# Performance work log

Hardware: AMD Instinct MI355X
Metric: run time of the kernel (lower is better)

## Reference

```python
import jax, jax.numpy as jnp
import numpy as np

N_HEAD = 16
EPS = 1e-5


def setup_inputs() -> dict:
    key = jax.random.key(0)
    ks = jax.random.split(key, 9)
    B, T, C = 2, 1024, 1024
    s = 0.02
    return {
        "x": jax.random.normal(ks[0], (B, T, C), jnp.float32),
        "Wq": jax.random.normal(ks[1], (C, C), jnp.float32) * s,
        "Wk": jax.random.normal(ks[2], (C, C), jnp.float32) * s,
        "Wv": jax.random.normal(ks[3], (C, C), jnp.float32) * s,
        "Wq2": jax.random.normal(ks[4], (C, C), jnp.float32) * s,
        "Wk2": jax.random.normal(ks[5], (C, C), jnp.float32) * s,
        "Wo": jax.random.normal(ks[6], (C, C), jnp.float32) * s,
        "mixture": jnp.full((1,), -5.0, jnp.float32),  # quartet_gate_init
        "quartet_scale": jnp.ones((1,), jnp.float32),
    }


def reference(x, Wq, Wk, Wv, Wq2, Wk2, Wo, mixture, quartet_scale):
    B, T, C = x.shape
    H = N_HEAD
    Dh = C // H
    scale = 1.0 / jnp.sqrt(jnp.asarray(Dh, x.dtype))

    def heads(W):
        # torch Linear: y = x @ W.T ; then view(B,T,H,Dh).transpose(1,2)
        return (x @ W.T).reshape(B, T, H, Dh).transpose(0, 2, 1, 3)  # [B,H,T,Dh]

    q, k, v = heads(Wq), heads(Wk), heads(Wv)
    q2, k2 = heads(Wq2), heads(Wk2)

    qk = jnp.einsum("bhqd,bhkd->bhqk", q, k) * scale      # [B,H,T,T]
    q2k2 = jnp.einsum("bhqd,bhkd->bhqk", q2, k2) * scale  # [B,H,T,T]

    def row_norm(s):
        mu = s.mean(axis=-1, keepdims=True)
        sigma = s.std(axis=-1, keepdims=True, ddof=1)  # torch std is unbiased
        return (s - mu) / (sigma + EPS)

    qk_n = row_norm(qk)
    q2k2_n = row_norm(q2k2)
    m = jax.nn.sigmoid(mixture)  # [1], broadcasts
    scores = (1.0 - m) * qk_n + m * (qk_n * q2k2_n) * quartet_scale

    causal = jnp.tril(jnp.ones((T, T), bool))  # [T,T]
    scores = jnp.where(causal, scores, -jnp.inf)
    attn = jax.nn.softmax(scores, axis=-1)  # [B,H,T,T]

    y = jnp.einsum("bhqk,bhkd->bhqd", attn, v)  # [B,H,T,Dh]
    y = y.transpose(0, 2, 1, 3).reshape(B, T, C)
    return y @ Wo.T
```

## Files before the change

kernel.cpp:

```cpp
#include <hip/hip_runtime.h>
#include <hip/hip_bf16.h>
#include <stdint.h>

#define TS 1024
#define CS 1024
#define NH 16
#define DHEAD 64
#define NBATCH 2
#define EPSV 1e-5f
#define MEG 1048576

typedef __bf16 bf16x8 __attribute__((ext_vector_type(8)));
typedef float  f32x4  __attribute__((ext_vector_type(4)));

#define MFMA(a, b, c) __builtin_amdgcn_mfma_f32_16x16x32_bf16((a), (b), (c), 0, 0, 0)

__device__ __forceinline__ float bf2f(ushort u){
  union { uint32_t i; float f; } v; v.i = ((uint32_t)u) << 16; return v.f;
}
__device__ __forceinline__ ushort f2bf(float f){
  union { float f; uint32_t i; } v; v.f = f;
  uint32_t r = v.i + 0x7FFFu + ((v.i >> 16) & 1u);
  return (ushort)(r >> 16);
}

__device__ __forceinline__ void gl_lds16(const ushort* g, ushort* l) {
  __builtin_amdgcn_global_load_lds(
      (const __attribute__((address_space(1))) void*)g,
      (__attribute__((address_space(3))) void*)l, 16, 0, 0);
}

__global__ __launch_bounds__(256)
void cast_all(const float* __restrict__ x,
              const float* __restrict__ Wq, const float* __restrict__ Wk,
              const float* __restrict__ Wv, const float* __restrict__ Wq2,
              const float* __restrict__ Wk2, const float* __restrict__ Wo,
              ushort* __restrict__ xb, ushort* __restrict__ wcat)
{
  const int XC = 524288, TOT = 2097152;
  for (int idx = blockIdx.x * 256 + threadIdx.x; idx < TOT; idx += 524288) {
    const float* s; ushort* d; int c;
    if (idx < XC) { s = x; d = xb; c = idx; }
    else {
      int r = idx - XC; int w = r >> 18; c = r & 262143;
      switch (w) {
        case 0:  s = Wq;  d = wcat;           break;
        case 1:  s = Wk;  d = wcat + 1*MEG;   break;
        case 2:  s = Wv;  d = wcat + 4*MEG;   break;
        case 3:  s = Wq2; d = wcat + 2*MEG;   break;
        case 4:  s = Wk2; d = wcat + 3*MEG;   break;
        default: s = Wo;  d = wcat + 5*MEG;   break;
      }
    }
    float4 v = *(const float4*)(s + (size_t)c * 4);
    ushort4 o; o.x = f2bf(v.x); o.y = f2bf(v.y); o.z = f2bf(v.z); o.w = f2bf(v.w);
    *(ushort4*)(d + (size_t)c * 4) = o;
  }
}

#define BN 128

__global__ __launch_bounds__(256, 2)
void gemm_proj(const ushort* __restrict__ A, const ushort* __restrict__ Bt,
               ushort* __restrict__ qb, ushort* __restrict__ kb,
               ushort* __restrict__ q2b, ushort* __restrict__ k2b,
               ushort* __restrict__ vtb,
               ushort* __restrict__ ktb, ushort* __restrict__ k2tb)
{
  __shared__ ushort a_s[64 * 64];
  __shared__ ushort b_s[128 * 64];

  const int bid = blockIdx.x;
  const int s   = (bid & 7) * 160 + (bid >> 3);
  const int n0  = (s >> 5) * BN;
  const int m0  = (s & 31) * 64;

  const int t  = threadIdx.x;
  const int w  = t >> 6, l = t & 63;
  const int wr = w >> 1, wc = w & 1;
  const int l15 = l & 15, l4 = l >> 4;
  const int r8 = l >> 3, g7 = l & 7;

  f32x4 acc[2][4] = {};

  for (int k0 = 0; k0 < CS; k0 += 64) {
    #pragma unroll
    for (int i = 0; i < 2; ++i) {
      int issue = w * 2 + i;
      int row   = issue * 8 + r8;
      int gs    = g7 ^ (row & 7);
      gl_lds16(&A[(size_t)(m0 + row) * CS + k0 + gs * 8], &a_s[issue * 512]);
    }
    #pragma unroll
    for (int i = 0; i < 4; ++i) {
      int issue = w * 4 + i;
      int row   = issue * 8 + r8;
      int gs    = g7 ^ (row & 7);
      gl_lds16(&Bt[(size_t)(n0 + row) * CS + k0 + gs * 8], &b_s[issue * 512]);
    }
    __syncthreads();

    #pragma unroll
    for (int ks = 0; ks < 2; ++ks) {
      bf16x8 af[2], bfr[4];
      #pragma unroll
      for (int mi = 0; mi < 2; ++mi) {
        int row = wr * 32 + mi * 16 + l15;
        int gl  = (ks * 4 + l4) ^ (row & 7);
        af[mi] = *(const bf16x8*)&a_s[row * 64 + gl * 8];
      }
      #pragma unroll
      for (int ni = 0; ni < 4; ++ni) {
        int row = wc * 64 + ni * 16 + l15;
        int gl  = (ks * 4 + l4) ^ (row & 7);
        bfr[ni] = *(const bf16x8*)&b_s[row * 64 + gl * 8];
      }
      #pragma unroll
      for (int mi = 0; mi < 2; ++mi)
        #pragma unroll
        for (int ni = 0; ni < 4; ++ni)
          acc[mi][ni] = MFMA(af[mi], bfr[ni], acc[mi][ni]);
    }

    __syncthreads();
  }

  #pragma unroll
  for (int mi = 0; mi < 2; ++mi) {
    #pragma unroll
    for (int ni = 0; ni < 4; ++ni) {
      int col  = n0 + wc * 64 + ni * 16 + l15;
      int row0 = m0 + wr * 32 + mi * 16 + l4 * 4;
      int seg  = col >> 10, cc = col & (CS - 1);
      if (seg < 4) {
        ushort* dst = (seg == 0) ? qb : (seg == 1) ? kb : (seg == 2) ? q2b : k2b;
        float sc = (seg & 1) ? 1.f : 0.125f;
        #pragma unroll
        for (int e = 0; e < 4; ++e)
          dst[(size_t)(row0 + e) * CS + cc] = f2bf(acc[mi][ni][e] * sc);
        if (seg == 1 || seg == 3) {
          int bb = row0 >> 10, tt = row0 & (TS - 1);
          int hh = cc >> 6, dd = cc & (DHEAD - 1);
          ushort* td = (seg == 1) ? ktb : k2tb;
          ushort4 o;
          o.x = f2bf(acc[mi][ni][0]); o.y = f2bf(acc[mi][ni][1]);
          o.z = f2bf(acc[mi][ni][2]); o.w = f2bf(acc[mi][ni][3]);
          *(ushort4*)&td[(((size_t)(bb * NH + hh) * DHEAD + dd) * TS) + tt] = o;
        }
      } else {
        int bb = row0 >> 10, tt = row0 & (TS - 1);
        int hh = cc >> 6, dd = cc & (DHEAD - 1);
        ushort4 o;
        o.x = f2bf(acc[mi][ni][0]); o.y = f2bf(acc[mi][ni][1]);
        o.z = f2bf(acc[mi][ni][2]); o.w = f2bf(acc[mi][ni][3]);
        *(ushort4*)&vtb[(((size_t)(bb * NH + hh) * DHEAD + dd) * TS) + tt] = o;
      }
    }
  }
}

__global__ __launch_bounds__(256, 2)
void gemm_out(const ushort* __restrict__ A, const ushort* __restrict__ Bt,
              float* __restrict__ C)
{
  __shared__ ushort a_s[64 * 64];
  __shared__ ushort b_s[64 * 64];

  const int bid = blockIdx.x;
  const int s   = (bid & 7) * 64 + (bid >> 3);
  const int n0  = (s >> 5) * 64;
  const int m0  = (s & 31) * 64;

  const int t  = threadIdx.x;
  const int w  = t >> 6, l = t & 63;
  const int wr = w >> 1, wc = w & 1;
  const int l15 = l & 15, l4 = l >> 4;
  const int r8 = l >> 3, g7 = l & 7;

  f32x4 acc[2][2] = {};

  for (int k0 = 0; k0 < CS; k0 += 64) {
    #pragma unroll
    for (int i = 0; i < 2; ++i) {
      int issue = w * 2 + i;
      int row   = issue * 8 + r8;
      int gs    = g7 ^ (row & 7);
      gl_lds16(&A [(size_t)(m0 + row) * CS + k0 + gs * 8], &a_s[issue * 512]);
      gl_lds16(&Bt[(size_t)(n0 + row) * CS + k0 + gs * 8], &b_s[issue * 512]);
    }
    __syncthreads();

    #pragma unroll
    for (int ks = 0; ks < 2; ++ks) {
      bf16x8 af[2], bfr[2];
      #pragma unroll
      for (int mi = 0; mi < 2; ++mi) {
        int row = wr * 32 + mi * 16 + l15;
        int gl  = (ks * 4 + l4) ^ (row & 7);
        af[mi] = *(const bf16x8*)&a_s[row * 64 + gl * 8];
      }
      #pragma unroll
      for (int ni = 0; ni < 2; ++ni) {
        int row = wc * 32 + ni * 16 + l15;
        int gl  = (ks * 4 + l4) ^ (row & 7);
        bfr[ni] = *(const bf16x8*)&b_s[row * 64 + gl * 8];
      }
      #pragma unroll
      for (int mi = 0; mi < 2; ++mi)
        #pragma unroll
        for (int ni = 0; ni < 2; ++ni)
          acc[mi][ni] = MFMA(af[mi], bfr[ni], acc[mi][ni]);
    }

    __syncthreads();
  }

  #pragma unroll
  for (int mi = 0; mi < 2; ++mi)
    #pragma unroll
    for (int ni = 0; ni < 2; ++ni)
      #pragma unroll
      for (int e = 0; e < 4; ++e)
        C[(size_t)(m0 + wr * 32 + mi * 16 + l4 * 4 + e) * CS +
          n0 + wc * 32 + ni * 16 + l15] = acc[mi][ni][e];
}

__global__ __launch_bounds__(256, 2)
void gram(const ushort* __restrict__ ktb, const ushort* __restrict__ k2tb,
          ushort* __restrict__ g1b, ushort* __restrict__ g2b,
          float* __restrict__ csb)
{
  __shared__ ushort t_s[64 * 128];

  const int mat = blockIdx.x & 1, z = blockIdx.x >> 1;
  const ushort* S = (mat ? k2tb : ktb) + (size_t)z * DHEAD * TS;

  const int t = threadIdx.x, w = t >> 6, l = t & 63;
  const int l15 = l & 15, l4 = l >> 4;

  f32x4 acc[4] = {};
  float csacc = 0.f;

  for (int tt = 0; tt < 8; ++tt) {
    const int t0 = tt * 128;
    __syncthreads();
    #pragma unroll
    for (int i = 0; i < 4; ++i) {
      int issue = w * 4 + i;
      int row = issue * 4 + l4;
      int gs  = l15 ^ (row & 15);
      gl_lds16(&S[(size_t)row * TS + t0 + gs * 8], &t_s[issue * 512]);
    }
    __syncthreads();

    {
      int r = w * 16 + l15;
      #pragma unroll
      for (int j = 0; j < 4; ++j) {
        int gg = ((l4 * 4 + j) ^ (r & 15)) * 8;
        uint4 vv = *(const uint4*)&t_s[r * 128 + gg];
        const ushort* pu = (const ushort*)&vv;
        #pragma unroll
        for (int e2 = 0; e2 < 8; ++e2) csacc += bf2f(pu[e2]);
      }
    }

    #pragma unroll
    for (int ks = 0; ks < 4; ++ks) {
      int ar = w * 16 + l15;
      bf16x8 af = *(const bf16x8*)&t_s[ar * 128 + ((ks * 4 + l4) ^ (ar & 15)) * 8];
      #pragma unroll
      for (int ni = 0; ni < 4; ++ni) {
        int br = ni * 16 + l15;
        bf16x8 bf_ = *(const bf16x8*)&t_s[br * 128 + ((ks * 4 + l4) ^ (br & 15)) * 8];
        acc[ni] = MFMA(af, bf_, acc[ni]);
      }
    }
  }

  csacc += __shfl_xor(csacc, 16);
  csacc += __shfl_xor(csacc, 32);
  if (l4 == 0)
    csb[(mat * 32 + z) * 64 + w * 16 + l15] = csacc;

  ushort* G = (mat ? g2b : g1b) + (size_t)z * 4096;
  #pragma unroll
  for (int ni = 0; ni < 4; ++ni)
    #pragma unroll
    for (int e = 0; e < 4; ++e)
      G[(w * 16 + l4 * 4 + e) * 64 + ni * 16 + l15] = f2bf(acc[ni][e]);
}

__global__ __launch_bounds__(256, 3)
void attn_fused(const ushort* __restrict__ qb, const ushort* __restrict__ kb,
                const ushort* __restrict__ q2b, const ushort* __restrict__ k2b,
                const ushort* __restrict__ vtb, ushort* __restrict__ yb,
                const ushort* __restrict__ g1b, const ushort* __restrict__ g2b,
                const float* __restrict__ csb,
                const float* __restrict__ mixture, const float* __restrict__ qsc)
{
  __shared__ ushort kbuf [2][4096];
  __shared__ ushort k2buf[2][4096];
  __shared__ ushort vbuf [2][4096];
  __shared__ ushort p_s  [2 * 32 * 40];

  const int idx  = blockIdx.x;
  const int pp   = idx >> 8;
  const int base = idx & 255;
  const int xcd  = base & 7;
  const int mm   = base >> 3;
  const int qq   = mm & 7;
  const int z    = (mm >> 3) * 8 + xcd;
  const int q32  = (pp == 0) ? (31 - qq) : (pp == 1) ? qq
                 : (pp == 2) ? (23 - qq) : (8 + qq);
  const int b    = z >> 4, h = z & 15;
  const int m0   = q32 * 32;
  const int nkv  = (q32 >> 1) + 1;

  const ushort* Q  = qb  + (size_t)b * TS * CS + h * DHEAD;
  const ushort* Q2 = q2b + (size_t)b * TS * CS + h * DHEAD;
  const ushort* K  = kb  + (size_t)b * TS * CS + h * DHEAD;
  const ushort* K2 = k2b + (size_t)b * TS * CS + h * DHEAD;
  const ushort* Vt = vtb + (size_t)z * DHEAD * TS;
  const ushort* G1 = g1b + (size_t)z * 4096;
  const ushort* G2 = g2b + (size_t)z * 4096;
  ushort* Y = yb + (size_t)b * TS * CS + h * DHEAD;

  const int t = threadIdx.x, w = t >> 6, l = t & 63;
  const int l15 = l & 15, l4 = l >> 4;
  const int r8 = l >> 3, g7 = l & 7;
  const int p  = w >> 1, wr = w & 1;
  const int qrow = wr * 16 + l15;

  const float L2E = 1.44269504f;
  const float gm = 1.f / (1.f + __expf(-mixture[0]));
  const float mq2 = gm * qsc[0] * L2E;
  const float om2 = (1.f - gm) * L2E;

  auto stage_k = [&](int ti, int bs) {
    const int t0 = ti * 64;
    #pragma unroll
    for (int i = 0; i < 2; ++i) {
      int issue = w * 2 + i;
      int row = issue * 8 + r8;
      int gs  = g7 ^ (row & 7);
      gl_lds16(&K [(size_t)(t0 + row) * CS + gs * 8], &kbuf [bs][issue * 512]);
      gl_lds16(&K2[(size_t)(t0 + row) * CS + gs * 8], &k2buf[bs][issue * 512]);
    }
  };
  auto stage_v = [&](int ti, int bs) {
    const int t0 = ti * 64;
    #pragma unroll
    for (int i = 0; i < 2; ++i) {
      int issue = w * 2 + i;
      int row = issue * 8 + r8;
      int gs  = g7 ^ (row & 7);
      gl_lds16(&Vt[(size_t)row * TS + t0 + gs * 8], &vbuf[bs][issue * 512]);
    }
  };

  {
    int row = w * 8 + r8;
    int gs  = g7 ^ (row & 7);
    gl_lds16(&Q [(size_t)(m0 + row) * CS + gs * 8], &p_s[w * 512]);
    gl_lds16(&Q2[(size_t)(m0 + row) * CS + gs * 8], &kbuf[1][w * 512]);
  }
  stage_k(0, 0);
  stage_v(0, 0);
  __syncthreads();

  bf16x8 fq[2], fq2[2];
  #pragma unroll
  for (int ks = 0; ks < 2; ++ks) {
    int gg = ((ks * 4 + l4) ^ (qrow & 7)) * 8;
    fq [ks] = *(const bf16x8*)&p_s[qrow * 64 + gg];
    fq2[ks] = *(const bf16x8*)&kbuf[1][qrow * 64 + gg];
  }

  f32x4 U1[4] = {}, U2[4] = {};
  #pragma unroll
  for (int ks = 0; ks < 2; ++ks)
    #pragma unroll
    for (int ni = 0; ni < 4; ++ni) {
      bf16x8 bg = *(const bf16x8*)&G1[(ni * 16 + l15) * 64 + ks * 32 + l4 * 8];
      U1[ni] = MFMA(bg, fq[ks], U1[ni]);
    }
  #pragma unroll
  for (int ks = 0; ks < 2; ++ks)
    #pragma unroll
    for (int ni = 0; ni < 4; ++ni) {
      bf16x8 bg = *(const bf16x8*)&G2[(ni * 16 + l15) * 64 + ks * 32 + l4 * 8];
      U2[ni] = MFMA(bg, fq2[ks], U2[ni]);
    }

  float ssq1 = 0.f, md1 = 0.f, ssq2 = 0.f, md2 = 0.f;
  #pragma unroll
  for (int ni = 0; ni < 4; ++ni) {
    int gsq = (ni * 2 + (l4 >> 1)) ^ (qrow & 7);
    int off = qrow * 64 + gsq * 8 + (l4 & 1) * 4;
    ushort qa[4], qb2[4];
    *(uint2*)qa  = *(const uint2*)&p_s[off];
    *(uint2*)qb2 = *(const uint2*)&kbuf[1][off];
    float c1[4], c2[4];
    *(float4*)c1 = *(const float4*)&csb[z * 64 + ni * 16 + l4 * 4];
    *(float4*)c2 = *(const float4*)&csb[2048 + z * 64 + ni * 16 + l4 * 4];
    #pragma unroll
    for (int e = 0; e < 4; ++e) {
      float qv1 = bf2f(qa[e]), qv2 = bf2f(qb2[e]);
      ssq1 = fmaf(U1[ni][e], qv1, ssq1); md1 = fmaf(qv1, c1[e], md1);
      ssq2 = fmaf(U2[ni][e], qv2, ssq2); md2 = fmaf(qv2, c2[e], md2);
    }
  }
  ssq1 += __shfl_xor(ssq1, 16); md1 += __shfl_xor(md1, 16);
  ssq2 += __shfl_xor(ssq2, 16); md2 += __shfl_xor(md2, 16);
  ssq1 += __shfl_xor(ssq1, 32); md1 += __shfl_xor(md1, 32);
  ssq2 += __shfl_xor(ssq2, 32); md2 += __shfl_xor(md2, 32);

  const float mu1 = md1 * (1.f / TS), mu2 = md2 * (1.f / TS);
  const float va1 = (ssq1 - (float)TS * mu1 * mu1) * (1.f / (TS - 1));
  const float va2 = (ssq2 - (float)TS * mu2 * mu2) * (1.f / (TS - 1));
  const float iv1 = 1.f / (sqrtf(fmaxf(va1, 0.f)) + EPSV);
  const float iv2 = 1.f / (sqrtf(fmaxf(va2, 0.f)) + EPSV);
  __syncthreads();

  float lrow = 0.f;
  f32x4 accO[4] = {};

  for (int i = 0; i < nkv; ++i) {
    const int t0  = i * 64;
    const int cur = i & 1;
    if (i + 1 < nkv) { stage_k(i + 1, cur ^ 1); stage_v(i + 1, cur ^ 1); }

    const ushort* ks_ = kbuf [cur];
    const ushort* k2s_= k2buf[cur];

    f32x4 a1[2] = {}, a2[2] = {};
    #pragma unroll
    for (int ks = 0; ks < 2; ++ks) {
      bf16x8 bk[2], bk2[2];
      #pragma unroll
      for (int ni = 0; ni < 2; ++ni) {
        int j  = p * 32 + ni * 16 + l15;
        int gg = ((ks * 4 + l4) ^ (j & 7)) * 8;
        bk [ni] = *(const bf16x8*)&ks_ [j * 64 + gg];
        bk2[ni] = *(const bf16x8*)&k2s_[j * 64 + gg];
      }
      #pragma unroll
      for (int ni = 0; ni < 2; ++ni) {
        a1[ni] = MFMA(bk [ni], fq [ks], a1[ni]);
        a2[ni] = MFMA(bk2[ni], fq2[ks], a2[ni]);
      }
    }

    const int grow = m0 + qrow;
    #pragma unroll
    for (int ni = 0; ni < 2; ++ni) {
      float pe[4];
      #pragma unroll
      for (int e = 0; e < 4; ++e) {
        float n1 = (a1[ni][e] - mu1) * iv1;
        float n2 = (a2[ni][e] - mu2) * iv2;
        float sc = n1 * fmaf(mq2, n2, om2);
        float pv = exp2f(sc);
        int gcol = t0 + p * 32 + ni * 16 + l4 * 4 + e;
        pv = (gcol <= grow) ? pv : 0.f;
        lrow += pv;
        pe[e] = pv;
      }
      uint32_t pk01, pk23;
      asm("v_cvt_pk_bf16_f32 %0, %1, %2" : "=v"(pk01) : "v"(pe[0]), "v"(pe[1]));
      asm("v_cvt_pk_bf16_f32 %0, %1, %2" : "=v"(pk23) : "v"(pe[2]), "v"(pe[3]));
      uint2 pk; pk.x = pk01; pk.y = pk23;
      *(uint2*)&p_s[p * 1280 + qrow * 40 + ni * 16 + l4 * 4] = pk;
    }

    {
      bf16x8 ap = *(const bf16x8*)&p_s[p * 1280 + qrow * 40 + l4 * 8];
      #pragma unroll
      for (int ni = 0; ni < 4; ++ni) {
        int d  = ni * 16 + l15;
        int gg = ((p * 4 + l4) ^ (d & 7)) * 8;
        bf16x8 bv = *(const bf16x8*)&vbuf[cur][d * 64 + gg];
        accO[ni] = MFMA(ap, bv, accO[ni]);
      }
    }

    __syncthreads();
  }

  lrow += __shfl_xor(lrow, 16);
  lrow += __shfl_xor(lrow, 32);

  float* fb = (float*)kbuf;
  float* fl = (float*)k2buf;
  if (p == 1) {
    #pragma unroll
    for (int ni = 0; ni < 4; ++ni)
      #pragma unroll
      for (int e = 0; e < 4; ++e)
        fb[(wr * 16 + l4 * 4 + e) * 64 + ni * 16 + l15] = accO[ni][e];
    if (l4 == 0) fl[qrow] = lrow;
  }
  __syncthreads();
  if (p == 0) {
    float lt = lrow + fl[qrow];
    float il[4];
    #pragma unroll
    for (int e = 0; e < 4; ++e)
      il[e] = 1.f / __shfl(lt, l4 * 4 + e);
    #pragma unroll
    for (int ni = 0; ni < 4; ++ni)
      #pragma unroll
      for (int e = 0; e < 4; ++e) {
        float o = accO[ni][e] + fb[(wr * 16 + l4 * 4 + e) * 64 + ni * 16 + l15];
        Y[(size_t)(m0 + wr * 16 + l4 * 4 + e) * CS + ni * 16 + l15] = f2bf(o * il[e]);
      }
  }
}

extern "C" void kernel_launch(void* const* d_in, const int* in_sizes, int n_in,
                              void* d_out, int out_size, void* d_ws, size_t ws_size,
                              hipStream_t stream) {
  const float* x    = (const float*)d_in[0];
  const float* Wq   = (const float*)d_in[1];
  const float* Wk   = (const float*)d_in[2];
  const float* Wv   = (const float*)d_in[3];
  const float* Wq2  = (const float*)d_in[4];
  const float* Wk2  = (const float*)d_in[5];
  const float* Wo   = (const float*)d_in[6];
  const float* mixture = (const float*)d_in[7];
  const float* qsc  = (const float*)d_in[8];
  float* out = (float*)d_out;

  ushort* ws = (ushort*)d_ws;
  ushort* xb   = ws;
  ushort* wcat = xb   + (size_t)2 * MEG;
  ushort* qb   = wcat + (size_t)6 * MEG;
  ushort* q2b  = qb   + (size_t)2 * MEG;
  ushort* kb   = q2b  + (size_t)2 * MEG;
  ushort* k2b  = kb   + (size_t)2 * MEG;
  ushort* vtb  = k2b  + (size_t)2 * MEG;
  ushort* yb   = vtb  + (size_t)2 * MEG;
  ushort* ktb  = yb   + (size_t)2 * MEG;
  ushort* k2tb = ktb  + (size_t)2 * MEG;
  ushort* g1b  = k2tb + (size_t)2 * MEG;
  ushort* g2b  = g1b  + (size_t)(MEG / 8);
  float*  csb  = (float*)(g2b + (size_t)(MEG / 8));
  ushort* wob  = wcat + (size_t)5 * MEG;

  cast_all<<<2048, 256, 0, stream>>>(x, Wq, Wk, Wv, Wq2, Wk2, Wo, xb, wcat);

  gemm_proj<<<1280, 256, 0, stream>>>(
      xb, wcat, qb, kb, q2b, k2b, vtb, ktb, k2tb);

  gram<<<64, 256, 0, stream>>>(ktb, k2tb, g1b, g2b, csb);

  attn_fused<<<1024, 256, 0, stream>>>(qb, kb, q2b, k2b, vtb, yb,
                                       g1b, g2b, csb, mixture, qsc);

  gemm_out<<<512, 256, 0, stream>>>(yb, wob, out);
}
```

Measured before the change: 105.5 us.

## Load K2 fragments directly into registers, drop K2 LDS staging

K2 tiles are no longer staged through shared memory; each wave loads its MFMA fragments straight from global memory into a double-buffered register set, and the KV loop is unrolled by two so the register buffers alternate statically. This cuts LDS footprint by a third, which can raise occupancy, and removes the LDS reads for K2. In exchange it raises register pressure and uses uncoalesced-ish direct global loads whose latency must be hidden by one tile of compute.

```diff
diff --git a/kernel.cpp b/kernel.cpp
--- a/kernel.cpp
+++ b/kernel.cpp
@@ -299,10 +299,9 @@
                 const float* __restrict__ csb,
                 const float* __restrict__ mixture, const float* __restrict__ qsc)
 {
-  __shared__ ushort kbuf [2][4096];
-  __shared__ ushort k2buf[2][4096];
-  __shared__ ushort vbuf [2][4096];
-  __shared__ ushort p_s  [2 * 32 * 40];
+  __shared__ ushort kbuf[2][4096];
+  __shared__ ushort vbuf[2][4096];
+  __shared__ ushort p_s [2 * 32 * 40];
 
   const int idx  = blockIdx.x;
   const int pp   = idx >> 8;
@@ -344,8 +343,7 @@
       int issue = w * 2 + i;
       int row = issue * 8 + r8;
       int gs  = g7 ^ (row & 7);
-      gl_lds16(&K [(size_t)(t0 + row) * CS + gs * 8], &kbuf [bs][issue * 512]);
-      gl_lds16(&K2[(size_t)(t0 + row) * CS + gs * 8], &k2buf[bs][issue * 512]);
+      gl_lds16(&K[(size_t)(t0 + row) * CS + gs * 8], &kbuf[bs][issue * 512]);
     }
   };
   auto stage_v = [&](int ti, int bs) {
@@ -359,6 +357,18 @@
     }
   };
 
+  bf16x8 k2A[2][2], k2B[2][2];
+#define LOAD_K2(ti, dst)                                                        \
+  {                                                                             \
+    const int t0_ = (ti) * 64;                                                  \
+    _Pragma("unroll")                                                           \
+    for (int ni = 0; ni < 2; ++ni)                                              \
+      _Pragma("unroll")                                                         \
+      for (int ks = 0; ks < 2; ++ks)                                            \
+        dst[ni][ks] = *(const bf16x8*)&K2[(size_t)(t0_ + p * 32 + ni * 16 + l15)\
+                                          * CS + ks * 32 + l4 * 8];             \
+  }
+
   {
     int row = w * 8 + r8;
     int gs  = g7 ^ (row & 7);
@@ -367,6 +377,7 @@
   }
   stage_k(0, 0);
   stage_v(0, 0);
+  LOAD_K2(0, k2A);
   __syncthreads();
 
   bf16x8 fq[2], fq2[2];
@@ -426,73 +437,82 @@
   float lrow = 0.f;
   f32x4 accO[4] = {};
 
-  for (int i = 0; i < nkv; ++i) {
-    const int t0  = i * 64;
-    const int cur = i & 1;
-    if (i + 1 < nkv) { stage_k(i + 1, cur ^ 1); stage_v(i + 1, cur ^ 1); }
-
-    const ushort* ks_ = kbuf [cur];
-    const ushort* k2s_= k2buf[cur];
-
-    f32x4 a1[2] = {}, a2[2] = {};
-    #pragma unroll
-    for (int ks = 0; ks < 2; ++ks) {
-      bf16x8 bk[2], bk2[2];
-      #pragma unroll
-      for (int ni = 0; ni < 2; ++ni) {
-        int j  = p * 32 + ni * 16 + l15;
-        int gg = ((ks * 4 + l4) ^ (j & 7)) * 8;
-        bk [ni] = *(const bf16x8*)&ks_ [j * 64 + gg];
-        bk2[ni] = *(const bf16x8*)&k2s_[j * 64 + gg];
-      }
-      #pragma unroll
-      for (int ni = 0; ni < 2; ++ni) {
-        a1[ni] = MFMA(bk [ni], fq [ks], a1[ni]);
-        a2[ni] = MFMA(bk2[ni], fq2[ks], a2[ni]);
-      }
-    }
-
-    const int grow = m0 + qrow;
-    #pragma unroll
-    for (int ni = 0; ni < 2; ++ni) {
-      float pe[4];
-      #pragma unroll
-      for (int e = 0; e < 4; ++e) {
-        float n1 = (a1[ni][e] - mu1) * iv1;
-        float n2 = (a2[ni][e] - mu2) * iv2;
-        float sc = n1 * fmaf(mq2, n2, om2);
-        float pv = exp2f(sc);
-        int gcol = t0 + p * 32 + ni * 16 + l4 * 4 + e;
-        pv = (gcol <= grow) ? pv : 0.f;
-        lrow += pv;
-        pe[e] = pv;
-      }
-      uint32_t pk01, pk23;
-      asm("v_cvt_pk_bf16_f32 %0, %1, %2" : "=v"(pk01) : "v"(pe[0]), "v"(pe[1]));
-      asm("v_cvt_pk_bf16_f32 %0, %1, %2" : "=v"(pk23) : "v"(pe[2]), "v"(pe[3]));
-      uint2 pk; pk.x = pk01; pk.y = pk23;
-      *(uint2*)&p_s[p * 1280 + qrow * 40 + ni * 16 + l4 * 4] = pk;
-    }
-
-    {
-      bf16x8 ap = *(const bf16x8*)&p_s[p * 1280 + qrow * 40 + l4 * 8];
-      #pragma unroll
-      for (int ni = 0; ni < 4; ++ni) {
-        int d  = ni * 16 + l15;
-        int gg = ((p * 4 + l4) ^ (d & 7)) * 8;
-        bf16x8 bv = *(const bf16x8*)&vbuf[cur][d * 64 + gg];
-        accO[ni] = MFMA(ap, bv, accO[ni]);
-      }
-    }
-
-    __syncthreads();
-  }
+#define COMPUTE_TILE(ti, KS_, VS_, K2F)                                         \
+  {                                                                             \
+    const int t0 = (ti) * 64;                                                   \
+    f32x4 a1[2] = {}, a2[2] = {};                                               \
+    _Pragma("unroll")                                                           \
+    for (int ks = 0; ks < 2; ++ks) {                                            \
+      bf16x8 bk[2];                                                             \
+      _Pragma("unroll")                                                         \
+      for (int ni = 0; ni < 2; ++ni) {                                          \
+        int j  = p * 32 + ni * 16 + l15;                                        \
+        int gg = ((ks * 4 + l4) ^ (j & 7)) * 8;                                 \
+        bk[ni] = *(const bf16x8*)&KS_[j * 64 + gg];                             \
+      }                                                                         \
+      _Pragma("unroll")                                                         \
+      for (int ni = 0; ni < 2; ++ni) {                                          \
+        a1[ni] = MFMA(bk[ni], fq[ks], a1[ni]);                                  \
+        a2[ni] = MFMA(K2F[ni][ks], fq2[ks], a2[ni]);                            \
+      }                                                                         \
+    }                                                                           \
+    const int grow = m0 + qrow;                                                 \
+    _Pragma("unroll")                                                           \
+    for (int ni = 0; ni < 2; ++ni) {                                            \
+      float pe[4];                                                              \
+      _Pragma("unroll")                                                         \
+      for (int e = 0; e < 4; ++e) {                                             \
+        float n1 = (a1[ni][e] - mu1) * iv1;                                     \
+        float n2 = (a2[ni][e] - mu2) * iv2;                                     \
+        float sc = n1 * fmaf(mq2, n2, om2);                                     \
+        float pv = exp2f(sc);                                                   \
+        int gcol = t0 + p * 32 + ni * 16 + l4 * 4 + e;                          \
+        pv = (gcol <= grow) ? pv : 0.f;                                         \
+        lrow += pv;                                                             \
+        pe[e] = pv;                                                             \
+      }                                                                         \
+      uint32_t pk01, pk23;                                                      \
+      asm("v_cvt_pk_bf16_f32 %0, %1, %2" : "=v"(pk01) : "v"(pe[0]), "v"(pe[1]));\
+      asm("v_cvt_pk_bf16_f32 %0, %1, %2" : "=v"(pk23) : "v"(pe[2]), "v"(pe[3]));\
+      uint2 pk; pk.x = pk01; pk.y = pk23;                                       \
+      *(uint2*)&p_s[p * 1280 + qrow * 40 + ni * 16 + l4 * 4] = pk;              \
+    }                                                                           \
+    {                                                                           \
+      bf16x8 ap = *(const bf16x8*)&p_s[p * 1280 + qrow * 40 + l4 * 8];          \
+      _Pragma("unroll")                                                         \
+      for (int ni = 0; ni < 4; ++ni) {                                          \
+        int d  = ni * 16 + l15;                                                 \
+        int gg = ((p * 4 + l4) ^ (d & 7)) * 8;                                  \
+        bf16x8 bv = *(const bf16x8*)&VS_[d * 64 + gg];                          \
+        accO[ni] = MFMA(ap, bv, accO[ni]);                                      \
+      }                                                                         \
+    }                                                                           \
+  }
+
+  for (int ii = 0; ii < nkv; ii += 2) {
+    if (ii + 1 < nkv) {
+      stage_k(ii + 1, 1); stage_v(ii + 1, 1);
+      LOAD_K2(ii + 1, k2B);
+    }
+    COMPUTE_TILE(ii, kbuf[0], vbuf[0], k2A);
+    __syncthreads();
+    if (ii + 1 >= nkv) break;
+
+    if (ii + 2 < nkv) {
+      stage_k(ii + 2, 0); stage_v(ii + 2, 0);
+      LOAD_K2(ii + 2, k2A);
+    }
+    COMPUTE_TILE(ii + 1, kbuf[1], vbuf[1], k2B);
+    __syncthreads();
+  }
+#undef COMPUTE_TILE
+#undef LOAD_K2
 
   lrow += __shfl_xor(lrow, 16);
   lrow += __shfl_xor(lrow, 32);
 
   float* fb = (float*)kbuf;
-  float* fl = (float*)k2buf;
+  float* fl = (float*)vbuf;
   if (p == 1) {
     #pragma unroll
     for (int ni = 0; ni < 4; ++ni)
```

Result: no change. 104.8 us (-0.6%).

## Use 64-row query tiles per attention block, dropping the KV split-reduction

Applied to the files above, without the earlier changes.

Each attention block now covers 64 query rows, one 16-row slice per wave, over the full 64-column KV tile, where before it covered 32 rows split across two wave pairs that each took half the KV columns. This halves the grid and removes the final cross-wave reduction through shared memory and its extra barrier. It also halves K/K2/V loads per query row, since each staged tile now serves twice as many rows. In exchange each wave holds twice the score accumulators, the launch bound drops to 2 blocks per CU, and fewer, longer blocks may balance less evenly over the causal workload.

```diff
diff --git a/kernel.cpp b/kernel.cpp
--- a/kernel.cpp
+++ b/kernel.cpp
@@ -291,7 +291,7 @@
       G[(w * 16 + l4 * 4 + e) * 64 + ni * 16 + l15] = f2bf(acc[ni][e]);
 }
 
-__global__ __launch_bounds__(256, 3)
+__global__ __launch_bounds__(256, 2)
 void attn_fused(const ushort* __restrict__ qb, const ushort* __restrict__ kb,
                 const ushort* __restrict__ q2b, const ushort* __restrict__ k2b,
                 const ushort* __restrict__ vtb, ushort* __restrict__ yb,
@@ -302,7 +302,7 @@
   __shared__ ushort kbuf [2][4096];
   __shared__ ushort k2buf[2][4096];
   __shared__ ushort vbuf [2][4096];
-  __shared__ ushort p_s  [2 * 32 * 40];
+  __shared__ ushort p_s  [64 * 72];
 
   const int idx  = blockIdx.x;
   const int pp   = idx >> 8;
@@ -311,11 +311,10 @@
   const int mm   = base >> 3;
   const int qq   = mm & 7;
   const int z    = (mm >> 3) * 8 + xcd;
-  const int q32  = (pp == 0) ? (31 - qq) : (pp == 1) ? qq
-                 : (pp == 2) ? (23 - qq) : (8 + qq);
+  const int q64  = pp ? qq : (15 - qq);
   const int b    = z >> 4, h = z & 15;
-  const int m0   = q32 * 32;
-  const int nkv  = (q32 >> 1) + 1;
+  const int m0   = q64 * 64;
+  const int nkv  = q64 + 1;
 
   const ushort* Q  = qb  + (size_t)b * TS * CS + h * DHEAD;
   const ushort* Q2 = q2b + (size_t)b * TS * CS + h * DHEAD;
@@ -329,8 +328,7 @@
   const int t = threadIdx.x, w = t >> 6, l = t & 63;
   const int l15 = l & 15, l4 = l >> 4;
   const int r8 = l >> 3, g7 = l & 7;
-  const int p  = w >> 1, wr = w & 1;
-  const int qrow = wr * 16 + l15;
+  const int qrow = w * 16 + l15;
 
   const float L2E = 1.44269504f;
   const float gm = 1.f / (1.f + __expf(-mixture[0]));
@@ -359,11 +357,13 @@
     }
   };
 
-  {
-    int row = w * 8 + r8;
+  #pragma unroll
+  for (int i = 0; i < 2; ++i) {
+    int issue = w * 2 + i;
+    int row = issue * 8 + r8;
     int gs  = g7 ^ (row & 7);
-    gl_lds16(&Q [(size_t)(m0 + row) * CS + gs * 8], &p_s[w * 512]);
-    gl_lds16(&Q2[(size_t)(m0 + row) * CS + gs * 8], &kbuf[1][w * 512]);
+    gl_lds16(&Q [(size_t)(m0 + row) * CS + gs * 8], &kbuf [1][issue * 512]);
+    gl_lds16(&Q2[(size_t)(m0 + row) * CS + gs * 8], &k2buf[1][issue * 512]);
   }
   stage_k(0, 0);
   stage_v(0, 0);
@@ -373,8 +373,8 @@
   #pragma unroll
   for (int ks = 0; ks < 2; ++ks) {
     int gg = ((ks * 4 + l4) ^ (qrow & 7)) * 8;
-    fq [ks] = *(const bf16x8*)&p_s[qrow * 64 + gg];
-    fq2[ks] = *(const bf16x8*)&kbuf[1][qrow * 64 + gg];
+    fq [ks] = *(const bf16x8*)&kbuf [1][qrow * 64 + gg];
+    fq2[ks] = *(const bf16x8*)&k2buf[1][qrow * 64 + gg];
   }
 
   f32x4 U1[4] = {}, U2[4] = {};
@@ -399,8 +399,8 @@
     int gsq = (ni * 2 + (l4 >> 1)) ^ (qrow & 7);
     int off = qrow * 64 + gsq * 8 + (l4 & 1) * 4;
     ushort qa[4], qb2[4];
-    *(uint2*)qa  = *(const uint2*)&p_s[off];
-    *(uint2*)qb2 = *(const uint2*)&kbuf[1][off];
+    *(uint2*)qa  = *(const uint2*)&kbuf [1][off];
+    *(uint2*)qb2 = *(const uint2*)&k2buf[1][off];
     float c1[4], c2[4];
     *(float4*)c1 = *(const float4*)&csb[z * 64 + ni * 16 + l4 * 4];
     *(float4*)c2 = *(const float4*)&csb[2048 + z * 64 + ni * 16 + l4 * 4];
@@ -434,19 +434,19 @@
     const ushort* ks_ = kbuf [cur];
     const ushort* k2s_= k2buf[cur];
 
-    f32x4 a1[2] = {}, a2[2] = {};
+    f32x4 a1[4] = {}, a2[4] = {};
     #pragma unroll
     for (int ks = 0; ks < 2; ++ks) {
-      bf16x8 bk[2], bk2[2];
-      #pragma unroll
-      for (int ni = 0; ni < 2; ++ni) {
-        int j  = p * 32 + ni * 16 + l15;
+      bf16x8 bk[4], bk2[4];
+      #pragma unroll
+      for (int ni = 0; ni < 4; ++ni) {
+        int j  = ni * 16 + l15;
         int gg = ((ks * 4 + l4) ^ (j & 7)) * 8;
         bk [ni] = *(const bf16x8*)&ks_ [j * 64 + gg];
         bk2[ni] = *(const bf16x8*)&k2s_[j * 64 + gg];
       }
       #pragma unroll
-      for (int ni = 0; ni < 2; ++ni) {
+      for (int ni = 0; ni < 4; ++ni) {
         a1[ni] = MFMA(bk [ni], fq [ks], a1[ni]);
         a2[ni] = MFMA(bk2[ni], fq2[ks], a2[ni]);
       }
@@ -454,7 +454,7 @@
 
     const int grow = m0 + qrow;
     #pragma unroll
-    for (int ni = 0; ni < 2; ++ni) {
+    for (int ni = 0; ni < 4; ++ni) {
       float pe[4];
       #pragma unroll
       for (int e = 0; e < 4; ++e) {
@@ -462,7 +462,7 @@
         float n2 = (a2[ni][e] - mu2) * iv2;
         float sc = n1 * fmaf(mq2, n2, om2);
         float pv = exp2f(sc);
-        int gcol = t0 + p * 32 + ni * 16 + l4 * 4 + e;
+        int gcol = t0 + ni * 16 + l4 * 4 + e;
         pv = (gcol <= grow) ? pv : 0.f;
         lrow += pv;
         pe[e] = pv;
@@ -471,15 +471,16 @@
       asm("v_cvt_pk_bf16_f32 %0, %1, %2" : "=v"(pk01) : "v"(pe[0]), "v"(pe[1]));
       asm("v_cvt_pk_bf16_f32 %0, %1, %2" : "=v"(pk23) : "v"(pe[2]), "v"(pe[3]));
       uint2 pk; pk.x = pk01; pk.y = pk23;
-      *(uint2*)&p_s[p * 1280 + qrow * 40 + ni * 16 + l4 * 4] = pk;
-    }
-
-    {
-      bf16x8 ap = *(const bf16x8*)&p_s[p * 1280 + qrow * 40 + l4 * 8];
+      *(uint2*)&p_s[qrow * 72 + ni * 16 + l4 * 4] = pk;
+    }
+
+    #pragma unroll
+    for (int ks = 0; ks < 2; ++ks) {
+      bf16x8 ap = *(const bf16x8*)&p_s[qrow * 72 + ks * 32 + l4 * 8];
       #pragma unroll
       for (int ni = 0; ni < 4; ++ni) {
         int d  = ni * 16 + l15;
-        int gg = ((p * 4 + l4) ^ (d & 7)) * 8;
+        int gg = ((ks * 4 + l4) ^ (d & 7)) * 8;
         bf16x8 bv = *(const bf16x8*)&vbuf[cur][d * 64 + gg];
         accO[ni] = MFMA(ap, bv, accO[ni]);
       }
@@ -490,32 +491,16 @@
 
   lrow += __shfl_xor(lrow, 16);
   lrow += __shfl_xor(lrow, 32);
-
-  float* fb = (float*)kbuf;
-  float* fl = (float*)k2buf;
-  if (p == 1) {
-    #pragma unroll
-    for (int ni = 0; ni < 4; ++ni)
-      #pragma unroll
-      for (int e = 0; e < 4; ++e)
-        fb[(wr * 16 + l4 * 4 + e) * 64 + ni * 16 + l15] = accO[ni][e];
-    if (l4 == 0) fl[qrow] = lrow;
-  }
-  __syncthreads();
-  if (p == 0) {
-    float lt = lrow + fl[qrow];
-    float il[4];
+  float il[4];
+  #pragma unroll
+  for (int e = 0; e < 4; ++e)
+    il[e] = 1.f / __shfl(lrow, l4 * 4 + e);
+  #pragma unroll
+  for (int ni = 0; ni < 4; ++ni)
     #pragma unroll
     for (int e = 0; e < 4; ++e)
-      il[e] = 1.f / __shfl(lt, l4 * 4 + e);
-    #pragma unroll
-    for (int ni = 0; ni < 4; ++ni)
-      #pragma unroll
-      for (int e = 0; e < 4; ++e) {
-        float o = accO[ni][e] + fb[(wr * 16 + l4 * 4 + e) * 64 + ni * 16 + l15];
-        Y[(size_t)(m0 + wr * 16 + l4 * 4 + e) * CS + ni * 16 + l15] = f2bf(o * il[e]);
-      }
-  }
+      Y[(size_t)(m0 + w * 16 + l4 * 4 + e) * CS + ni * 16 + l15] =
+          f2bf(accO[ni][e] * il[e]);
 }
 
 extern "C" void kernel_launch(void* const* d_in, const int* in_sizes, int n_in,
@@ -555,8 +540,8 @@
 
   gram<<<64, 256, 0, stream>>>(ktb, k2tb, g1b, g2b, csb);
 
-  attn_fused<<<1024, 256, 0, stream>>>(qb, kb, q2b, k2b, vtb, yb,
-                                       g1b, g2b, csb, mixture, qsc);
+  attn_fused<<<512, 256, 0, stream>>>(qb, kb, q2b, k2b, vtb, yb,
+                                      g1b, g2b, csb, mixture, qsc);
 
   gemm_out<<<512, 256, 0, stream>>>(yb, wob, out);
 }
```

Result: faster. 99.57 us, median of 2 (-5.6%).
